# Optimization experiments

Measured on AMD Instinct MI355X. Metric: run time of the kernel, lower is better.

## Reference

```python
import jax, jax.numpy as jnp
import numpy as np

MAX_DIST = 32  # unidirectional T5-style bucketing: num_buckets = 33
N_HEAD, D_K, D_V = 8, 64, 64


def setup_inputs() -> dict:
    key = jax.random.key(0)
    ks = jax.random.split(key, 9)
    B, S, D = 4, 2048, 512
    q = jax.random.normal(ks[0], (B, S, D), dtype=jnp.float32)
    k = jax.random.normal(ks[1], (B, S, D), dtype=jnp.float32)
    v = jax.random.normal(ks[2], (B, S, D), dtype=jnp.float32)
    mask = jax.random.randint(ks[3], (B, 1, 1, S), 0, 2, dtype=jnp.int32)
    sc = 1.0 / np.sqrt(D)
    Wq = jax.random.normal(ks[4], (D, D), dtype=jnp.float32) * sc
    Wk = jax.random.normal(ks[5], (D, D), dtype=jnp.float32) * sc
    Wv = jax.random.normal(ks[6], (D, D), dtype=jnp.float32) * sc
    Wfc = jax.random.normal(ks[7], (D, D), dtype=jnp.float32) * sc
    rel_bias = jax.random.normal(ks[8], (MAX_DIST + 1, N_HEAD), dtype=jnp.float32)
    return {"q": q, "k": k, "v": v, "mask": mask, "Wq": Wq, "Wk": Wk,
            "Wv": Wv, "Wfc": Wfc, "rel_bias": rel_bias}


def _rel_pos_bias(rel_bias, seq_len):
    # unidirectional: bucket = clamp(max(context - memory, 0), 0, MAX_DIST)
    pos = jnp.arange(seq_len)
    n = pos[:, None] - pos[None, :]              # context - memory = -relative_position
    bucket = jnp.clip(jnp.maximum(n, 0), 0, MAX_DIST)
    vals = rel_bias[bucket]                      # (S, S, H)
    return jnp.transpose(vals, (2, 0, 1))[None]  # (1, H, S, S)


def reference(q, k, v, mask, Wq, Wk, Wv, Wfc, rel_bias):
    B, Sq, _ = q.shape
    Sk = k.shape[1]
    scale = D_K ** (-0.5)
    qh = (q @ Wq).reshape(B, Sq, N_HEAD, D_K).transpose(0, 2, 1, 3)  # bhsd
    kh = (k @ Wk).reshape(B, Sk, N_HEAD, D_K).transpose(0, 2, 1, 3)
    vh = (v @ Wv).reshape(B, Sk, N_HEAD, D_V).transpose(0, 2, 1, 3)
    attn = jnp.einsum('bhqd,bhkd->bhqk', qh, kh) * scale
    attn = attn + _rel_pos_bias(rel_bias, Sq)
    attn = jnp.where(mask == 0, jnp.float32(-1e9), attn)
    attn = jax.nn.softmax(attn, axis=-1)          # dropout is identity at eval
    out = jnp.einsum('bhqk,bhkd->bhqd', attn, vh)
    out = out.transpose(0, 2, 1, 3).reshape(B, Sq, N_HEAD * D_V)
    out = out @ Wfc
    return out, attn
```

## Files before the change

### kernel.cpp

```cpp
#include <hip/hip_runtime.h>


typedef __attribute__((ext_vector_type(8))) short bfrag;
typedef __attribute__((ext_vector_type(4))) float f32x4;
typedef unsigned int u32;

#define MFMA16(a,b,c) __builtin_amdgcn_mfma_f32_16x16x32_bf16(a,b,c,0,0,0)

__device__ __forceinline__ void gl_lds16(const void* g, void* l){
  __builtin_amdgcn_global_load_lds((const __attribute__((address_space(1))) u32*)g,
                                   (__attribute__((address_space(3))) u32*)l, 16, 0, 0);
}
__device__ __forceinline__ short f2bs(float f){
  u32 u = __float_as_uint(f);
  u = (u + 0x7fffu + ((u>>16)&1u)) >> 16;
  return (short)u;
}
__device__ __forceinline__ float b2f(short s){
  return __uint_as_float(((u32)(unsigned short)s) << 16);
}

#define BB 4
#define HH 8
#define SS 2048
#define DD 512

#define WQT_OFF  0u
#define WKT_OFF  524288u
#define WVT_OFF  1048576u
#define WFCT_OFF 1572864u
#define QB_OFF   2097152u
#define KB_OFF   10485760u
#define VB_OFF   18874368u
#define QH_OFF   27262976u
#define KH_OFF   35651584u
#define VT_OFF   44040192u
#define OH_OFF   52428800u

__global__ __launch_bounds__(256) void conv_w_k(const float* w0,const float* w1,
                                                const float* w2,const float* w3, char* ws){
  const float* w; short* o;
  switch(blockIdx.z){
    case 0:  w=w0; o=(short*)(ws+WQT_OFF); break;
    case 1:  w=w1; o=(short*)(ws+WKT_OFF); break;
    case 2:  w=w2; o=(short*)(ws+WVT_OFF); break;
    default: w=w3; o=(short*)(ws+WFCT_OFF); break;
  }
  int t  = blockIdx.x*256 + threadIdx.x;
  int n  = t >> 6;
  int k0 = (t & 63) << 3;
  bfrag v;
  #pragma unroll
  for (int j=0;j<8;++j) v[j] = f2bs(w[(k0+j)*512 + n]);
  *(bfrag*)(o + n*512 + k0) = v;
}

__global__ __launch_bounds__(256) void conv_x_k(const float* x0,const float* x1,
                                                const float* x2, char* ws){
  const float* x; short* o;
  switch(blockIdx.z){
    case 0:  x=x0; o=(short*)(ws+QB_OFF); break;
    case 1:  x=x1; o=(short*)(ws+KB_OFF); break;
    default: x=x2; o=(short*)(ws+VB_OFF); break;
  }
  int i = (blockIdx.x*256 + threadIdx.x) << 3;
  float4 a = *(const float4*)(x+i);
  float4 b = *(const float4*)(x+i+4);
  bfrag v;
  v[0]=f2bs(a.x); v[1]=f2bs(a.y); v[2]=f2bs(a.z); v[3]=f2bs(a.w);
  v[4]=f2bs(b.x); v[5]=f2bs(b.y); v[6]=f2bs(b.z); v[7]=f2bs(b.w);
  *(bfrag*)(o+i) = v;
}

__device__ void gemm_core(const short* A, const short* Bt, char* Cout, int mode, int bid){
  __shared__ __align__(16) char lds[32768];
  int i0, j0;
  if (mode==1){ i0 = (bid&3)<<7; j0 = (bid>>2)<<7; }
  else        { i0 = (bid>>2)<<7; j0 = (bid&3)<<7; }
  int tid = threadIdx.x;
  int l = tid & 63, w = tid >> 6;
  int wr = (w>>1)<<6, wc = (w&1)<<6;
  int l15 = l & 15, l4 = l >> 4;
  f32x4 acc[4][4];
  #pragma unroll
  for(int a=0;a<4;++a)
    #pragma unroll
    for(int b=0;b<4;++b) acc[a][b] = (f32x4){0.f,0.f,0.f,0.f};
  const char* Ab = (const char*)A;
  const char* Bb = (const char*)Bt;
  for (int kk=0; kk<8; ++kk){
    #pragma unroll
    for (int it=0; it<4; ++it){
      int ci = it*256 + tid;
      int row = ci>>3, cc = ci&7;
      gl_lds16(Ab + (size_t)(i0+row)*1024 + kk*128 + ((cc^(row&7))<<4),
               lds + ((it*256 + w*64)<<4));
      gl_lds16(Bb + (size_t)(j0+row)*1024 + kk*128 + ((cc^(row&7))<<4),
               lds + 16384 + ((it*256 + w*64)<<4));
    }
    asm volatile("s_waitcnt vmcnt(0)" ::: "memory");
    __syncthreads();
    #pragma unroll
    for (int kb=0; kb<2; ++kb){
      bfrag af[4], bf[4];
      #pragma unroll
      for (int mi=0;mi<4;++mi){
        int row = wr + mi*16 + l15;
        af[mi] = *(const bfrag*)(lds + row*128 + (((kb*4 + l4) ^ (row&7))<<4));
      }
      #pragma unroll
      for (int ni=0;ni<4;++ni){
        int row = wc + ni*16 + l15;
        bf[ni] = *(const bfrag*)(lds + 16384 + row*128 + (((kb*4 + l4) ^ (row&7))<<4));
      }
      #pragma unroll
      for (int mi=0;mi<4;++mi)
        #pragma unroll
        for (int ni=0;ni<4;++ni)
          acc[mi][ni] = MFMA16(af[mi], bf[ni], acc[mi][ni]);
    }
    __syncthreads();
  }
  #pragma unroll
  for (int mi=0;mi<4;++mi){
    #pragma unroll
    for (int ni=0;ni<4;++ni){
      #pragma unroll
      for (int r=0;r<4;++r){
        int i = i0 + wr + mi*16 + (l4<<2) + r;
        int j = j0 + wc + ni*16 + l15;
        float v = acc[mi][ni][r];
        if (mode==2){
          ((float*)Cout)[(size_t)i*512 + j] = v;
        } else if (mode==0){
          size_t o = ((size_t)(((i>>11)<<3) + (j>>6))*2048 + (size_t)(i&2047))*64 + (j&63);
          ((short*)Cout)[o] = f2bs(v);
        } else {
          size_t o = ((size_t)(((j>>11)<<3) + (i>>6))*64 + (size_t)(i&63))*2048 + (j&2047);
          ((short*)Cout)[o] = f2bs(v);
        }
      }
    }
  }
}

__global__ __launch_bounds__(256,2) void gemm_proj_k(char* ws){
  switch(blockIdx.z){
    case 0:  gemm_core((const short*)(ws+QB_OFF),  (const short*)(ws+WQT_OFF), ws+QH_OFF, 0, blockIdx.x); break;
    case 1:  gemm_core((const short*)(ws+KB_OFF),  (const short*)(ws+WKT_OFF), ws+KH_OFF, 0, blockIdx.x); break;
    default: gemm_core((const short*)(ws+WVT_OFF), (const short*)(ws+VB_OFF),  ws+VT_OFF, 1, blockIdx.x); break;
  }
}
__global__ __launch_bounds__(256,2) void gemm_final_k(char* ws, float* out){
  gemm_core((const short*)(ws+OH_OFF), (const short*)(ws+WFCT_OFF), (char*)out, 2, blockIdx.x);
}

#define MSK_OFF_L   131072
#define BIAS_OFF_L  139264
#define WSUM_OFF_L  139424
#define RECIP_OFF_L 140448
#define LDS_TOTAL   140576

__global__ __launch_bounds__(512,1) void attn_k(char* ws, const int* mask,
                                                const float* rel_bias, float* attn_out){
  extern __shared__ __align__(16) char sm[];
  int tid = threadIdx.x;
  int l = tid & 63, w = tid >> 6;
  int l15 = l & 15, l4 = l >> 4;
  int bh = blockIdx.x, qblk = blockIdx.y;
  int b = bh >> 3, h = bh & 7;
  const short* qhb = (const short*)(ws+QH_OFF) + (size_t)bh*SS*64;
  const char*  khb = ws + KH_OFF + (size_t)bh*SS*128;
  const char*  vtb = ws + VT_OFF + (size_t)bh*64*SS*2;

  {
    const int4* m4 = (const int4*)(mask + b*SS);
    int4 ma = m4[tid];
    float4* mf = (float4*)(sm + MSK_OFF_L);
    mf[tid] = make_float4(ma.x?1.f:0.f, ma.y?1.f:0.f, ma.z?1.f:0.f, ma.w?1.f:0.f);
  }
  if (tid < 33) ((float*)(sm+BIAS_OFF_L))[tid] = rel_bias[tid*HH + h];

  int qrow = (qblk<<5) + l15;
  bfrag qA0 = *(const bfrag*)(qhb + (size_t)qrow*64 + l4*8);
  bfrag qA1 = *(const bfrag*)(qhb + (size_t)qrow*64 + 32 + l4*8);
  bfrag qB0 = *(const bfrag*)(qhb + (size_t)(qrow+16)*64 + l4*8);
  bfrag qB1 = *(const bfrag*)(qhb + (size_t)(qrow+16)*64 + 32 + l4*8);
  const float* biasl = (const float*)(sm+BIAS_OFF_L);
  const float* maskl = (const float*)(sm+MSK_OFF_L);
  float rsum[8] = {0.f,0.f,0.f,0.f,0.f,0.f,0.f,0.f};

  __syncthreads();

  int wbase = w << 8;
  #pragma unroll 2
  for (int t=0; t<16; ++t){
    int rowk = wbase + (t<<4) + l15;
    const char* kr = khb + (size_t)rowk*128 + (l4<<4);
    bfrag b0 = *(const bfrag*)(kr);
    bfrag b1 = *(const bfrag*)(kr + 64);
    f32x4 acc0 = (f32x4){0.f,0.f,0.f,0.f};
    f32x4 acc1 = (f32x4){0.f,0.f,0.f,0.f};
    acc0 = MFMA16(qA0, b0, acc0);
    acc0 = MFMA16(qA1, b1, acc0);
    acc1 = MFMA16(qB0, b0, acc1);
    acc1 = MFMA16(qB1, b1, acc1);
    float mval = maskl[rowk];
    int rl0 = l4<<2;
    int byte = rowk<<1;
    #pragma unroll
    for (int hf=0; hf<2; ++hf){
      f32x4 acc = hf ? acc1 : acc0;
      #pragma unroll
      for (int r=0;r<4;++r){
        int rowl = (hf<<4) + rl0 + r;
        int n = (qblk<<5) + rowl - rowk;
        n = n<0 ? 0 : (n>32 ? 32 : n);
        float s = acc[r]*0.125f + biasl[n];
        float p = mval * __expf(s);
        rsum[(hf<<2)+r] += p;
        int ch = (byte>>4) ^ (rowl&15);
        *(short*)(sm + rowl*4096 + (ch<<4) + (byte&15)) = f2bs(p);
      }
    }
  }

  {
    float* wsum = (float*)(sm+WSUM_OFF_L);
    #pragma unroll
    for (int i=0;i<8;++i){
      float s = rsum[i];
      s += __shfl_xor(s,1); s += __shfl_xor(s,2);
      s += __shfl_xor(s,4); s += __shfl_xor(s,8);
      if (l15==0){
        int rowl = ((i>>2)<<4) + (l4<<2) + (i&3);
        wsum[(w<<5) + rowl] = s;
      }
    }
  }
  __syncthreads();
  if (tid < 32){
    float* wsum = (float*)(sm+WSUM_OFF_L);
    float t = 0.f;
    #pragma unroll
    for (int i=0;i<8;++i) t += wsum[(i<<5) + tid];
    ((float*)(sm+RECIP_OFF_L))[tid] = 1.f/t;
  }
  __syncthreads();
  const float* recip = (const float*)(sm+RECIP_OFF_L);

  f32x4 acco = (f32x4){0.f,0.f,0.f,0.f};
  int wq = w >> 2, dbase = (w&3)<<4;
  int prow = (wq<<4) + l15;
  int drow = dbase + l15;
  const char* vr = vtb + (size_t)drow*4096 + (l4<<4);
  #pragma unroll 4
  for (int vc=0; vc<64; ++vc){
    int ch = ((vc<<2) + l4) ^ l15;
    bfrag af = *(const bfrag*)(sm + prow*4096 + (ch<<4));
    bfrag bv = *(const bfrag*)(vr + (vc<<6));
    acco = MFMA16(af, bv, acco);
  }

  {
    short* oh = (short*)(ws + OH_OFF);
    #pragma unroll
    for (int r=0;r<4;++r){
      int rowl = (wq<<4) + (l4<<2) + r;
      float rc = recip[rowl];
      size_t sg = (size_t)b*SS + (qblk<<5) + rowl;
      oh[sg*512 + h*64 + dbase + l15] = f2bs(acco[r]*rc);
    }
  }

  {
    float* dst0 = attn_out + (size_t)bh*SS*SS + (size_t)(qblk<<5)*SS;
    #pragma unroll
    for (int rr=0; rr<4; ++rr){
      int rowl = (w<<2) + rr;
      float rc = recip[rowl];
      float* dst = dst0 + (size_t)rowl*SS;
      #pragma unroll
      for (int it=0; it<4; ++it){
        int col = it*512 + (l<<3);
        int ch = (col>>3) ^ (rowl&15);
        bfrag pv = *(const bfrag*)(sm + rowl*4096 + (ch<<4));
        f32x4 o0 = (f32x4){b2f(pv[0])*rc, b2f(pv[1])*rc, b2f(pv[2])*rc, b2f(pv[3])*rc};
        f32x4 o1 = (f32x4){b2f(pv[4])*rc, b2f(pv[5])*rc, b2f(pv[6])*rc, b2f(pv[7])*rc};
        __builtin_nontemporal_store(o0, (f32x4*)(dst+col));
        __builtin_nontemporal_store(o1, (f32x4*)(dst+col+4));
      }
    }
  }
}

extern "C" void kernel_launch(void* const* d_in, const int* in_sizes, int n_in,
                              void* d_out, int out_size, void* d_ws, size_t ws_size,
                              hipStream_t stream){
  const float* q   = (const float*)d_in[0];
  const float* k   = (const float*)d_in[1];
  const float* v   = (const float*)d_in[2];
  const int*  mask = (const int*)  d_in[3];
  const float* Wq  = (const float*)d_in[4];
  const float* Wk  = (const float*)d_in[5];
  const float* Wv  = (const float*)d_in[6];
  const float* Wfc = (const float*)d_in[7];
  const float* rb  = (const float*)d_in[8];
  char* ws = (char*)d_ws;
  float* out  = (float*)d_out;
  float* attn = out + (size_t)BB*SS*512;

  (void)hipFuncSetAttribute((const void*)attn_k,
        hipFuncAttributeMaxDynamicSharedMemorySize, LDS_TOTAL);

  conv_w_k<<<dim3(128,1,4), 256, 0, stream>>>(Wq, Wk, Wv, Wfc, ws);
  conv_x_k<<<dim3(2048,1,3), 256, 0, stream>>>(q, k, v, ws);
  gemm_proj_k<<<dim3(256,1,3), 256, 0, stream>>>(ws);
  attn_k<<<dim3(32,64), 512, LDS_TOTAL, stream>>>(ws, mask, rb, attn);
  gemm_final_k<<<dim3(256,1,1), 256, 0, stream>>>(ws, out);
}
```

Baseline: 397.5 us.

## Halve attention query tile to 16 rows and split PV over key halves

The attention kernel now handles 16 query rows per block instead of 32. This halves the LDS probability buffer (about 78KB instead of 140KB), which should let two blocks fit per CU, and it doubles the grid. In the P·V phase the 8 waves now split the key dimension into two halves and combine their partial sums through LDS with an extra barrier. The trade-offs are that K is reloaded twice as often per query row and each block pays more reduction and synchronisation overhead.

```diff
diff --git a/kernel.cpp b/kernel.cpp
--- a/kernel.cpp
+++ b/kernel.cpp
@@ -155,11 +155,12 @@
   gemm_core((const short*)(ws+OH_OFF), (const short*)(ws+WFCT_OFF), (char*)out, 2, blockIdx.x);
 }
 
-#define MSK_OFF_L   131072
-#define BIAS_OFF_L  139264
-#define WSUM_OFF_L  139424
-#define RECIP_OFF_L 140448
-#define LDS_TOTAL   140576
+#define MSK_OFF_L   65536
+#define BIAS_OFF_L  73728
+#define WSUM_OFF_L  73872
+#define RECIP_OFF_L 74384
+#define PVRED_OFF_L 74448
+#define LDS_TOTAL   78592
 
 __global__ __launch_bounds__(512,1) void attn_k(char* ws, const int* mask,
                                                 const float* rel_bias, float* attn_out){
@@ -181,14 +182,12 @@
   }
   if (tid < 33) ((float*)(sm+BIAS_OFF_L))[tid] = rel_bias[tid*HH + h];
 
-  int qrow = (qblk<<5) + l15;
+  int qrow = (qblk<<4) + l15;
   bfrag qA0 = *(const bfrag*)(qhb + (size_t)qrow*64 + l4*8);
   bfrag qA1 = *(const bfrag*)(qhb + (size_t)qrow*64 + 32 + l4*8);
-  bfrag qB0 = *(const bfrag*)(qhb + (size_t)(qrow+16)*64 + l4*8);
-  bfrag qB1 = *(const bfrag*)(qhb + (size_t)(qrow+16)*64 + 32 + l4*8);
   const float* biasl = (const float*)(sm+BIAS_OFF_L);
   const float* maskl = (const float*)(sm+MSK_OFF_L);
-  float rsum[8] = {0.f,0.f,0.f,0.f,0.f,0.f,0.f,0.f};
+  float rsum[4] = {0.f,0.f,0.f,0.f};
 
   __syncthreads();
 
@@ -199,91 +198,86 @@
     const char* kr = khb + (size_t)rowk*128 + (l4<<4);
     bfrag b0 = *(const bfrag*)(kr);
     bfrag b1 = *(const bfrag*)(kr + 64);
-    f32x4 acc0 = (f32x4){0.f,0.f,0.f,0.f};
-    f32x4 acc1 = (f32x4){0.f,0.f,0.f,0.f};
-    acc0 = MFMA16(qA0, b0, acc0);
-    acc0 = MFMA16(qA1, b1, acc0);
-    acc1 = MFMA16(qB0, b0, acc1);
-    acc1 = MFMA16(qB1, b1, acc1);
+    f32x4 acc = (f32x4){0.f,0.f,0.f,0.f};
+    acc = MFMA16(qA0, b0, acc);
+    acc = MFMA16(qA1, b1, acc);
     float mval = maskl[rowk];
     int rl0 = l4<<2;
     int byte = rowk<<1;
     #pragma unroll
-    for (int hf=0; hf<2; ++hf){
-      f32x4 acc = hf ? acc1 : acc0;
-      #pragma unroll
-      for (int r=0;r<4;++r){
-        int rowl = (hf<<4) + rl0 + r;
-        int n = (qblk<<5) + rowl - rowk;
-        n = n<0 ? 0 : (n>32 ? 32 : n);
-        float s = acc[r]*0.125f + biasl[n];
-        float p = mval * __expf(s);
-        rsum[(hf<<2)+r] += p;
-        int ch = (byte>>4) ^ (rowl&15);
-        *(short*)(sm + rowl*4096 + (ch<<4) + (byte&15)) = f2bs(p);
-      }
+    for (int r=0;r<4;++r){
+      int rowl = rl0 + r;
+      int n = (qblk<<4) + rowl - rowk;
+      n = n<0 ? 0 : (n>32 ? 32 : n);
+      float s = acc[r]*0.125f + biasl[n];
+      float p = mval * __expf(s);
+      rsum[r] += p;
+      int ch = (byte>>4) ^ rowl;
+      *(short*)(sm + rowl*4096 + (ch<<4) + (byte&15)) = f2bs(p);
     }
   }
 
   {
     float* wsum = (float*)(sm+WSUM_OFF_L);
     #pragma unroll
-    for (int i=0;i<8;++i){
-      float s = rsum[i];
+    for (int r=0;r<4;++r){
+      float s = rsum[r];
       s += __shfl_xor(s,1); s += __shfl_xor(s,2);
       s += __shfl_xor(s,4); s += __shfl_xor(s,8);
-      if (l15==0){
-        int rowl = ((i>>2)<<4) + (l4<<2) + (i&3);
-        wsum[(w<<5) + rowl] = s;
-      }
+      if (l15==0) wsum[(w<<4) + (l4<<2) + r] = s;
     }
   }
   __syncthreads();
-  if (tid < 32){
+  if (tid < 16){
     float* wsum = (float*)(sm+WSUM_OFF_L);
     float t = 0.f;
     #pragma unroll
-    for (int i=0;i<8;++i) t += wsum[(i<<5) + tid];
+    for (int i=0;i<8;++i) t += wsum[(i<<4) + tid];
     ((float*)(sm+RECIP_OFF_L))[tid] = 1.f/t;
   }
   __syncthreads();
   const float* recip = (const float*)(sm+RECIP_OFF_L);
 
   f32x4 acco = (f32x4){0.f,0.f,0.f,0.f};
-  int wq = w >> 2, dbase = (w&3)<<4;
-  int prow = (wq<<4) + l15;
-  int drow = dbase + l15;
-  const char* vr = vtb + (size_t)drow*4096 + (l4<<4);
+  int dbase = (w&3)<<4;
+  int khalf = w>>2;
+  int chbase = khalf<<7;
+  const char* vr = vtb + (size_t)(dbase + l15)*4096 + (khalf<<11) + (l4<<4);
   #pragma unroll 4
-  for (int vc=0; vc<64; ++vc){
-    int ch = ((vc<<2) + l4) ^ l15;
-    bfrag af = *(const bfrag*)(sm + prow*4096 + (ch<<4));
+  for (int vc=0; vc<32; ++vc){
+    int ch = (chbase + (vc<<2) + l4) ^ l15;
+    bfrag af = *(const bfrag*)(sm + l15*4096 + (ch<<4));
     bfrag bv = *(const bfrag*)(vr + (vc<<6));
     acco = MFMA16(af, bv, acco);
   }
-
   {
-    short* oh = (short*)(ws + OH_OFF);
-    #pragma unroll
-    for (int r=0;r<4;++r){
-      int rowl = (wq<<4) + (l4<<2) + r;
-      float rc = recip[rowl];
-      size_t sg = (size_t)b*SS + (qblk<<5) + rowl;
-      oh[sg*512 + h*64 + dbase + l15] = f2bs(acco[r]*rc);
+    f32x4* pvred = (f32x4*)(sm+PVRED_OFF_L);
+    if (w >= 4) pvred[((w-4)<<6) + l] = acco;
+    __syncthreads();
+    if (w < 4){
+      acco += pvred[(w<<6) + l];
+      short* oh = (short*)(ws + OH_OFF);
+      #pragma unroll
+      for (int r=0;r<4;++r){
+        int rowl = (l4<<2) + r;
+        float rc = recip[rowl];
+        size_t sg = (size_t)b*SS + (qblk<<4) + rowl;
+        oh[sg*512 + h*64 + dbase + l15] = f2bs(acco[r]*rc);
+      }
     }
   }
 
   {
-    float* dst0 = attn_out + (size_t)bh*SS*SS + (size_t)(qblk<<5)*SS;
-    #pragma unroll
-    for (int rr=0; rr<4; ++rr){
-      int rowl = (w<<2) + rr;
+    float* dst0 = attn_out + (size_t)bh*SS*SS + (size_t)(qblk<<4)*SS;
+    #pragma unroll
+    for (int rr=0; rr<2; ++rr){
+      int rowl = (w<<1) + rr;
       float rc = recip[rowl];
       float* dst = dst0 + (size_t)rowl*SS;
       #pragma unroll
       for (int it=0; it<4; ++it){
         int col = it*512 + (l<<3);
-        int ch = (col>>3) ^ (rowl&15);
+        int ch = (col>>3) ^ rowl;
         bfrag pv = *(const bfrag*)(sm + rowl*4096 + (ch<<4));
         f32x4 o0 = (f32x4){b2f(pv[0])*rc, b2f(pv[1])*rc, b2f(pv[2])*rc, b2f(pv[3])*rc};
         f32x4 o1 = (f32x4){b2f(pv[4])*rc, b2f(pv[5])*rc, b2f(pv[6])*rc, b2f(pv[7])*rc};
@@ -316,6 +310,6 @@
   conv_w_k<<<dim3(128,1,4), 256, 0, stream>>>(Wq, Wk, Wv, Wfc, ws);
   conv_x_k<<<dim3(2048,1,3), 256, 0, stream>>>(q, k, v, ws);
   gemm_proj_k<<<dim3(256,1,3), 256, 0, stream>>>(ws);
-  attn_k<<<dim3(32,64), 512, LDS_TOTAL, stream>>>(ws, mask, rb, attn);
+  attn_k<<<dim3(32,128), 512, LDS_TOTAL, stream>>>(ws, mask, rb, attn);
   gemm_final_k<<<dim3(256,1,1), 256, 0, stream>>>(ws, out);
 }
```

Result: faster. 371.5 us (-6.5%).
